# Optimization experiments

Hardware: AMD Instinct MI355X
Metric: run time of the kernel (lower is better)

## Reference

```python
import jax, jax.numpy as jnp
import numpy as np

B, N, D, H = 4, 1024, 1024, 16
Dh = D // H


def setup_inputs() -> dict:
    key = jax.random.key(0)
    ks = jax.random.split(key, 5)
    w = 0.02
    return {
        "x": jax.random.normal(ks[0], (B, N, D), dtype=jnp.float32),
        "Wq": jax.random.normal(ks[1], (D, D), dtype=jnp.float32) * w,
        "bq": jnp.zeros((D,), dtype=jnp.float32),
        "Wk": jax.random.normal(ks[2], (D, D), dtype=jnp.float32) * w,
        "bk": jnp.zeros((D,), dtype=jnp.float32),
        "Wv": jax.random.normal(ks[3], (D, D), dtype=jnp.float32) * w,
        "bv": jnp.zeros((D,), dtype=jnp.float32),
        "Wc": jax.random.normal(ks[4], (D, D), dtype=jnp.float32) * w,
        "bc": jnp.zeros((D,), dtype=jnp.float32),
    }


def reference(x, Wq, bq, Wk, bk, Wv, bv, Wc, bc):
    # q/k/v projections: nn.Linear computes x @ W.T + b
    q = jnp.einsum("bnd,ed->bne", x, Wq) + bq
    k = jnp.einsum("bnd,ed->bne", x, Wk) + bk
    v = jnp.einsum("bnd,ed->bne", x, Wv) + bv
    # split heads: [B,N,D] -> [B,H,N,Dh]
    qh = q.reshape(B, N, H, Dh).transpose(0, 2, 1, 3)
    kh = k.reshape(B, N, H, Dh).transpose(0, 2, 1, 3)
    vh = v.reshape(B, N, H, Dh).transpose(0, 2, 1, 3)
    # NOTE (faithful quirk): original uses scale = q.size(1) = seq_len N,
    # not head_dim, so scores are scaled by N**-0.5.
    scale = jnp.float32(N) ** -0.5
    scores = jnp.einsum("bhnd,bhmd->bhnm", qh, kh) * scale  # [B,H,N,N]
    attn = jax.nn.softmax(scores, axis=-1)
    # attn_dropout = 0.0 -> identity
    o = jnp.einsum("bhnm,bhmd->bhnd", attn, vh)  # [B,H,N,Dh]
    # NOTE (faithful quirk): original does v.resize(original_size) on the
    # contiguous [B,H,N,Dh] tensor, reinterpreting memory as [B,N,D]
    # WITHOUT permuting heads back. Replicate exactly:
    o = o.reshape(B, N, D)
    out = jnp.einsum("bnd,ed->bne", o, Wc) + bc
    return out
```

## Files before the change

### kernel.cpp

```cpp
#include <hip/hip_runtime.h>
#include <cstddef>
#include <cstdint>

#define B_  4
#define N_  1024
#define D_  1024
#define H_  16
#define DH  64
#define M_  4096

#define SC2 0.04508422f

typedef __attribute__((ext_vector_type(4)))  float   f32x4;
typedef __attribute__((ext_vector_type(16))) float   f32x16;
typedef __attribute__((ext_vector_type(8)))  __bf16  bf16x8;
typedef __attribute__((ext_vector_type(4)))  unsigned int u32x4;

#define MFMA(a, b, c)   __builtin_amdgcn_mfma_f32_16x16x32_bf16((a), (b), (c), 0, 0, 0)
#define MFMA32(a, b, c) __builtin_amdgcn_mfma_f32_32x32x16_bf16((a), (b), (c), 0, 0, 0)
#define GLDS(gp, lp) __builtin_amdgcn_global_load_lds( \
    (__attribute__((address_space(1))) void*)(gp),     \
    (__attribute__((address_space(3))) void*)(lp), 16, 0, 0)

static __device__ __forceinline__ unsigned cvtpk(float lo, float hi) {
    unsigned r;
    asm("v_cvt_pk_bf16_f32 %0, %1, %2" : "=v"(r) : "v"(lo), "v"(hi));
    return r;
}

__global__ __launch_bounds__(256) void convert_k(
    const float* __restrict__ x,  const float* __restrict__ Wq,
    const float* __restrict__ Wk, const float* __restrict__ Wv,
    const float* __restrict__ Wc,
    __bf16* __restrict__ xb, __bf16* __restrict__ wqkvb,
    __bf16* __restrict__ wcb)
{
    const unsigned u = blockIdx.x * 256u + threadIdx.x;
    const unsigned e = u * 8u;
    const float* src;
    __bf16* dst;
    if (e < 4194304u) { src = x + e; dst = xb + e; }
    else {
        const unsigned t2 = e - 4194304u;
        const unsigned wsel = t2 >> 20;
        const unsigned wo = t2 & 1048575u;
        src = (wsel == 0 ? Wq : wsel == 1 ? Wk : wsel == 2 ? Wv : Wc) + wo;
        dst = (wsel < 3 ? wqkvb + (size_t)wsel * 1048576u : wcb) + wo;
    }
    const float4 f0 = *(const float4*)(src);
    const float4 f1 = *(const float4*)(src + 4);
    bf16x8 r;
    r[0] = (__bf16)f0.x; r[1] = (__bf16)f0.y; r[2] = (__bf16)f0.z; r[3] = (__bf16)f0.w;
    r[4] = (__bf16)f1.x; r[5] = (__bf16)f1.y; r[6] = (__bf16)f1.z; r[7] = (__bf16)f1.w;
    *(bf16x8*)dst = r;
}

__global__ __launch_bounds__(512, 2) void gemm_qkv256(
    const __bf16* __restrict__ xb, const __bf16* __restrict__ Wb,
    const float* __restrict__ bq, const float* __restrict__ bk,
    const float* __restrict__ bv,
    __bf16* __restrict__ qk_out, __bf16* __restrict__ vT)
{
    __shared__ __bf16 ring[65536];

    const int tid  = threadIdx.x;
    const int w    = tid >> 6;
    const int lane = tid & 63;
    const int quad = lane >> 4;
    const int l15  = lane & 15;
    const int wr   = w >> 2;
    const int wc   = w & 3;

    const int bid = blockIdx.x;
    const bool VT = (bid >= 128);
    const int xcd = bid & 7;
    int m0, n0;
    const __bf16 *Ap, *Bp;
    if (!VT) {
        const int i  = bid >> 3;
        const int mt = (xcd >> 1) * 4 + (i >> 2);
        const int nt = (xcd & 1) * 4 + (i & 3);
        m0 = mt * 256; n0 = nt * 256;
        Ap = xb; Bp = Wb;
    } else {
        const int i  = (bid - 128) >> 3;
        m0 = (i & 3) * 256;
        n0 = (xcd * 2 + (i >> 2)) * 256;
        Ap = Wb + (size_t)2 * D_ * D_; Bp = xb;
    }

    const size_t sgl = (size_t)(w * 16 + l15) * D_ + quad * 8;
    const __bf16* Asrc = Ap + (size_t)m0 * D_ + sgl;
    const __bf16* Bsrc = Bp + (size_t)n0 * D_ + sgl;
    __bf16* const ringA = ring;
    __bf16* const ringB = ring + 32768;
    const int sdst = w * 1024;

#define STG_A(tt, h) do {                                               \
    const __bf16* s_ = Asrc + (size_t)(h) * 128 * D_ + (tt) * 64;       \
    __bf16* d_ = ringA + ((((tt) & 1) * 2 + (h)) * 8192) + sdst;        \
    GLDS(s_, d_); GLDS(s_ + 32, d_ + 512); } while (0)
#define STG_B(tt, h) do {                                               \
    const __bf16* s_ = Bsrc + (size_t)(h) * 128 * D_ + (tt) * 64;       \
    __bf16* d_ = ringB + ((((tt) & 1) * 2 + (h)) * 8192) + sdst;        \
    GLDS(s_, d_); GLDS(s_ + 32, d_ + 512); } while (0)

    f32x4 acc[8][4];
    #pragma unroll
    for (int i = 0; i < 8; ++i)
        #pragma unroll
        for (int j = 0; j < 4; ++j)
            acc[i][j] = (f32x4){0.f, 0.f, 0.f, 0.f};

    STG_B(0, 0); STG_B(0, 1);
    STG_A(0, 0); STG_A(0, 1);
    STG_B(1, 0); STG_B(1, 1);

    const int rdo = lane * 8;

#define READ_A(q)                                                       \
    afr[0][0] = *(const bf16x8*)(Asl + ((2*(q)  )*2 + 0)*512);          \
    afr[0][1] = *(const bf16x8*)(Asl + ((2*(q)  )*2 + 1)*512);          \
    afr[1][0] = *(const bf16x8*)(Asl + ((2*(q)+1)*2 + 0)*512);          \
    afr[1][1] = *(const bf16x8*)(Asl + ((2*(q)+1)*2 + 1)*512);

#define PHASE_MFMA(q)                                                   \
    __builtin_amdgcn_s_barrier();                                       \
    asm volatile("s_waitcnt lgkmcnt(0)" ::: "memory");                  \
    __builtin_amdgcn_s_setprio(1);                                      \
    _Pragma("unroll")                                                   \
    for (int i = 0; i < 2; ++i)                                         \
      _Pragma("unroll")                                                 \
      for (int nt = 0; nt < 4; ++nt) {                                  \
        acc[2*(q)+i][nt] = MFMA(afr[i][0], bfr[nt][0], acc[2*(q)+i][nt]); \
        acc[2*(q)+i][nt] = MFMA(afr[i][1], bfr[nt][1], acc[2*(q)+i][nt]); \
      }                                                                 \
    __builtin_amdgcn_s_setprio(0);

    for (int t = 0; t < 16; ++t) {
        if (t < 15) asm volatile("s_waitcnt vmcnt(4)" ::: "memory");
        else        asm volatile("s_waitcnt vmcnt(0)" ::: "memory");
        __builtin_amdgcn_s_barrier();

        const __bf16* Asl = ringA + ((t & 1) * 2 + wr) * 8192 + rdo;
        const __bf16* Bsl = ringB + ((t & 1) * 2 + (wc >> 1)) * 8192
                                  + (wc & 1) * 4096 + rdo;
        bf16x8 afr[2][2], bfr[4][2];

        if (t < 15) { STG_A(t + 1, 0); STG_A(t + 1, 1); }
        #pragma unroll
        for (int nt = 0; nt < 4; ++nt) {
            bfr[nt][0] = *(const bf16x8*)(Bsl + (nt * 2 + 0) * 512);
            bfr[nt][1] = *(const bf16x8*)(Bsl + (nt * 2 + 1) * 512);
        }
        READ_A(0)
        PHASE_MFMA(0)
        __builtin_amdgcn_s_barrier();

        if (t < 14) STG_B(t + 2, 0);
        READ_A(1)
        PHASE_MFMA(1)
        __builtin_amdgcn_s_barrier();

        if (t < 14) STG_B(t + 2, 1);
        READ_A(2)
        PHASE_MFMA(2)
        __builtin_amdgcn_s_barrier();

        READ_A(3)
        PHASE_MFMA(3)
    }
#undef STG_A
#undef STG_B
#undef READ_A
#undef PHASE_MFMA

    if (!VT) {
        const int zq = n0 >> 10;
        const float* bias = zq ? bk : bq;
        const float qs = zq ? 1.0f : SC2;
        const int nb = (n0 & 1023) + wc * 64;
        float bvv[4];
        #pragma unroll
        for (int nt = 0; nt < 4; ++nt) bvv[nt] = bias[nb + nt * 16 + l15];
        __bf16* C = qk_out + (size_t)zq * M_ * D_;
        #pragma unroll
        for (int mt = 0; mt < 8; ++mt) {
            #pragma unroll
            for (int r = 0; r < 4; ++r) {
                const int row = m0 + wr * 128 + mt * 16 + quad * 4 + r;
                #pragma unroll
                for (int nt = 0; nt < 4; ++nt) {
                    const int col = nb + nt * 16 + l15;
                    const size_t idx = (((size_t)(row >> 10) * H_ + (col >> 6)) * N_
                                        + (row & 1023)) * DH + (col & 63);
                    C[idx] = (__bf16)((acc[mt][nt][r] + bvv[nt]) * qs);
                }
            }
        }
    } else {
        #pragma unroll
        for (int mt = 0; mt < 8; ++mt) {
            #pragma unroll
            for (int r = 0; r < 4; ++r) {
                const int row = m0 + wr * 128 + mt * 16 + quad * 4 + r;
                const float brow = bv[row];
                #pragma unroll
                for (int nt = 0; nt < 4; ++nt) {
                    const int col = n0 + wc * 64 + nt * 16 + l15;
                    const size_t idx = (((size_t)(col >> 10) * H_ + (row >> 6)) * DH
                                        + (row & 63)) * N_ + (col & 1023);
                    vT[idx] = (__bf16)(acc[mt][nt][r] + brow);
                }
            }
        }
    }
}

__global__ __launch_bounds__(256, 6) void gemm_out(
    const __bf16* __restrict__ A0, const __bf16* __restrict__ Wb,
    const float* __restrict__ b0, float* __restrict__ Cb)
{
    __shared__ __bf16 As[2048];
    __shared__ __bf16 Bs[4096];

    const int tid  = threadIdx.x;
    const int w    = tid >> 6;
    const int lane = tid & 63;
    const int quad = lane >> 4;
    const int l15  = lane & 15;
    const int wr   = w >> 1, wc = w & 1;

    const int m0 = blockIdx.y * 64;
    const int n0 = blockIdx.x * 128;

    const int Tt = tid >> 6, ko = (tid >> 4) & 3, l = tid & 15;
    const size_t aoff  = (size_t)(m0 + Tt * 16 + l) * D_ + ko * 8;
    const size_t boff1 = (size_t)(n0 + Tt * 16 + l) * D_ + ko * 8;
    const size_t boff2 = boff1 + (size_t)64 * D_;
    __bf16* adst  = As + w * 512;
    __bf16* bdst1 = Bs + w * 512;
    __bf16* bdst2 = Bs + 2048 + w * 512;

    f32x4 acc[2][4];
    #pragma unroll
    for (int i = 0; i < 2; ++i)
        #pragma unroll
        for (int j = 0; j < 4; ++j)
            acc[i][j] = (f32x4){0.f, 0.f, 0.f, 0.f};

    for (int k0 = 0; k0 < D_; k0 += 32) {
        GLDS(A0 + aoff  + k0, adst);
        GLDS(Wb + boff1 + k0, bdst1);
        GLDS(Wb + boff2 + k0, bdst2);
        __syncthreads();

        bf16x8 af[2], bf[4];
        #pragma unroll
        for (int mt = 0; mt < 2; ++mt)
            af[mt] = *(const bf16x8*)(As + (((wr * 2 + mt) * 4 + quad) * 16 + l15) * 8);
        #pragma unroll
        for (int nt = 0; nt < 4; ++nt)
            bf[nt] = *(const bf16x8*)(Bs + (((wc * 4 + nt) * 4 + quad) * 16 + l15) * 8);
        #pragma unroll
        for (int mt = 0; mt < 2; ++mt)
            #pragma unroll
            for (int nt = 0; nt < 4; ++nt)
                acc[mt][nt] = MFMA(af[mt], bf[nt], acc[mt][nt]);
        __syncthreads();
    }

    float bvv[4];
    #pragma unroll
    for (int nt = 0; nt < 4; ++nt)
        bvv[nt] = b0[n0 + wc * 64 + nt * 16 + l15];
    #pragma unroll
    for (int mt = 0; mt < 2; ++mt) {
        #pragma unroll
        for (int r = 0; r < 4; ++r) {
            const int row = m0 + (wr * 2 + mt) * 16 + quad * 4 + r;
            #pragma unroll
            for (int nt = 0; nt < 4; ++nt) {
                const int col = n0 + wc * 64 + nt * 16 + l15;
                Cb[(size_t)row * D_ + col] = acc[mt][nt][r] + bvv[nt];
            }
        }
    }
}

__global__ __launch_bounds__(256, 2) void attn_mfma(
    const __bf16* __restrict__ qh, const __bf16* __restrict__ kh,
    const __bf16* __restrict__ vT, __bf16* __restrict__ ob)
{
    __shared__ __align__(16) __bf16 Ks[4096];
    __shared__ __align__(16) __bf16 Vs[4096];

    const int tid  = threadIdx.x;
    const int w    = tid >> 6;
    const int lane = tid & 63;
    const int la31 = lane & 31;
    const int hi   = lane >> 5;

    const int bh = blockIdx.x >> 3;
    const int qt = blockIdx.x & 7;
    const int b  = bh >> 4;
    const int h  = bh & 15;

    const size_t headQ = (size_t)(b * H_ + h) * N_;

    const int qrow = qt * 128 + w * 32 + la31;
    const __bf16* qp = qh + (headQ + qrow) * DH + hi * 8;
    const bf16x8 qf0 = *(const bf16x8*)(qp);
    const bf16x8 qf1 = *(const bf16x8*)(qp + 16);
    const bf16x8 qf2 = *(const bf16x8*)(qp + 32);
    const bf16x8 qf3 = *(const bf16x8*)(qp + 48);

    const __bf16* khead = kh + headQ * DH;
    const __bf16* vhead = vT + (size_t)(b * H_ + h) * DH * N_;

    const size_t koff0 = (size_t)la31 * DH + w * 16 + hi * 8;
    const size_t koff1 = koff0 + (size_t)32 * DH;
    const size_t voff0 = (size_t)((w & 1) * 32 + la31) * N_ + (w >> 1) * 16 + hi * 8;
    const size_t voff1 = voff0 + 32;
    __bf16* const kd0 = Ks + tid * 8;
    __bf16* const kd1 = Ks + tid * 8 + 2048;
    __bf16* const vd0 = Vs + tid * 8;
    __bf16* const vd1 = Vs + tid * 8 + 2048;

    f32x16 Ov0, Ov1;
    #pragma unroll
    for (int r = 0; r < 16; ++r) { Ov0[r] = 0.f; Ov1[r] = 0.f; }
    float psum = 0.f;

    bf16x8 kr0 = *(const bf16x8*)(khead + koff0);
    bf16x8 kr1 = *(const bf16x8*)(khead + koff1);
    bf16x8 vr0 = *(const bf16x8*)(vhead + voff0);
    bf16x8 vr1 = *(const bf16x8*)(vhead + voff1);

#define PACK(earr, base, dst) do {                                        \
    unsigned U_ = cvtpk(earr[(base) + 0], earr[(base) + 1]);              \
    unsigned W_ = cvtpk(earr[(base) + 2], earr[(base) + 3]);              \
    unsigned V_ = cvtpk(earr[(base) + 4], earr[(base) + 5]);              \
    unsigned Z_ = cvtpk(earr[(base) + 6], earr[(base) + 7]);              \
    asm volatile("v_permlane32_swap_b32 %0, %1" : "+v"(U_), "+v"(V_));    \
    asm volatile("v_permlane32_swap_b32 %0, %1" : "+v"(W_), "+v"(Z_));    \
    u32x4 pw_ = {U_, W_, V_, Z_};                                         \
    dst = __builtin_bit_cast(bf16x8, pw_);                                \
} while (0)

    for (int kt = 0; kt < 16; ++kt) {
        asm volatile("s_waitcnt lgkmcnt(0)" ::: "memory");
        __builtin_amdgcn_s_barrier();
        __builtin_amdgcn_sched_barrier(0);

        *(bf16x8*)kd0 = kr0;
        *(bf16x8*)kd1 = kr1;
        *(bf16x8*)vd0 = vr0;
        *(bf16x8*)vd1 = vr1;
        if (kt < 15) {
            const __bf16* kp = khead + (size_t)(kt + 1) * 64 * DH;
            const __bf16* vp = vhead + (size_t)(kt + 1) * 64;
            kr0 = *(const bf16x8*)(kp + koff0);
            kr1 = *(const bf16x8*)(kp + koff1);
            vr0 = *(const bf16x8*)(vp + voff0);
            vr1 = *(const bf16x8*)(vp + voff1);
        }
        asm volatile("s_waitcnt lgkmcnt(0)" ::: "memory");
        __builtin_amdgcn_s_barrier();
        __builtin_amdgcn_sched_barrier(0);

        f32x16 sa0, sa1;
        __builtin_amdgcn_s_setprio(1);
        {
            f32x16 z;
            #pragma unroll
            for (int r = 0; r < 16; ++r) z[r] = 0.f;
            bf16x8 kf;
            kf = *(const bf16x8*)(Ks + 0 * 512 + lane * 8); sa0 = MFMA32(kf, qf0, z);
            kf = *(const bf16x8*)(Ks + 1 * 512 + lane * 8); sa0 = MFMA32(kf, qf1, sa0);
            kf = *(const bf16x8*)(Ks + 2 * 512 + lane * 8); sa0 = MFMA32(kf, qf2, sa0);
            kf = *(const bf16x8*)(Ks + 3 * 512 + lane * 8); sa0 = MFMA32(kf, qf3, sa0);
            kf = *(const bf16x8*)(Ks + 4 * 512 + lane * 8); sa1 = MFMA32(kf, qf0, z);
            kf = *(const bf16x8*)(Ks + 5 * 512 + lane * 8); sa1 = MFMA32(kf, qf1, sa1);
            kf = *(const bf16x8*)(Ks + 6 * 512 + lane * 8); sa1 = MFMA32(kf, qf2, sa1);
            kf = *(const bf16x8*)(Ks + 7 * 512 + lane * 8); sa1 = MFMA32(kf, qf3, sa1);
        }
        __builtin_amdgcn_s_setprio(0);

        float e0[16], e1[16];
        #pragma unroll
        for (int r = 0; r < 16; ++r) { e0[r] = __builtin_exp2f(sa0[r]); psum += e0[r]; }
        #pragma unroll
        for (int r = 0; r < 16; ++r) { e1[r] = __builtin_exp2f(sa1[r]); psum += e1[r]; }

        bf16x8 pf0, pf1, pf2, pf3;
        PACK(e0, 0, pf0);
        PACK(e0, 8, pf1);
        PACK(e1, 0, pf2);
        PACK(e1, 8, pf3);

        __builtin_amdgcn_s_setprio(1);
        {
            bf16x8 vf;
            vf = *(const bf16x8*)(Vs + 0 * 512 + lane * 8); Ov0 = MFMA32(pf0, vf, Ov0);
            vf = *(const bf16x8*)(Vs + 2 * 512 + lane * 8); Ov0 = MFMA32(pf1, vf, Ov0);
            vf = *(const bf16x8*)(Vs + 4 * 512 + lane * 8); Ov0 = MFMA32(pf2, vf, Ov0);
            vf = *(const bf16x8*)(Vs + 6 * 512 + lane * 8); Ov0 = MFMA32(pf3, vf, Ov0);
            vf = *(const bf16x8*)(Vs + 1 * 512 + lane * 8); Ov1 = MFMA32(pf0, vf, Ov1);
            vf = *(const bf16x8*)(Vs + 3 * 512 + lane * 8); Ov1 = MFMA32(pf1, vf, Ov1);
            vf = *(const bf16x8*)(Vs + 5 * 512 + lane * 8); Ov1 = MFMA32(pf2, vf, Ov1);
            vf = *(const bf16x8*)(Vs + 7 * 512 + lane * 8); Ov1 = MFMA32(pf3, vf, Ov1);
        }
        __builtin_amdgcn_s_setprio(0);
    }
#undef PACK

    psum += __shfl_xor(psum, 32);
    const float inv = 1.0f / psum;

    __bf16* const obase = ob + (headQ + qt * 128 + w * 32) * DH;
    #pragma unroll
    for (int r = 0; r < 16; ++r) {
        const int q_r = (r & 3) + 8 * (r >> 2) + 4 * hi;
        const float ivr = __shfl(inv, q_r);
        __bf16* op = obase + (size_t)q_r * DH + la31;
        op[0]  = (__bf16)(Ov0[r] * ivr);
        op[32] = (__bf16)(Ov1[r] * ivr);
    }
}

extern "C" void kernel_launch(void* const* d_in, const int* in_sizes, int n_in,
                              void* d_out, int out_size, void* d_ws, size_t ws_size,
                              hipStream_t stream) {
    const float* x  = (const float*)d_in[0];
    const float* Wq = (const float*)d_in[1];
    const float* bq = (const float*)d_in[2];
    const float* Wk = (const float*)d_in[3];
    const float* bk = (const float*)d_in[4];
    const float* Wv = (const float*)d_in[5];
    const float* bv = (const float*)d_in[6];
    const float* Wc = (const float*)d_in[7];
    const float* bc = (const float*)d_in[8];
    float* out = (float*)d_out;

    char* base = (char*)d_ws;
    __bf16* xb    = (__bf16*)(base);
    __bf16* wqkvb = (__bf16*)(base + (size_t)8  * 1048576);
    __bf16* wcb   = (__bf16*)(base + (size_t)14 * 1048576);
    __bf16* qkvb  = (__bf16*)(base + (size_t)16 * 1048576);
    __bf16* vTb   = (__bf16*)(base + (size_t)40 * 1048576);
    __bf16* obf   = (__bf16*)(base);

    __bf16* qhb = qkvb;
    __bf16* khb = qkvb + (size_t)M_ * D_;

    convert_k<<<dim3(4096), dim3(256), 0, stream>>>(
        x, Wq, Wk, Wv, Wc, xb, wqkvb, wcb);

    gemm_qkv256<<<dim3(192), dim3(512), 0, stream>>>(
        xb, wqkvb, bq, bk, bv, qkvb, vTb);

    attn_mfma<<<dim3(512), dim3(256), 0, stream>>>(qhb, khb, vTb, obf);

    gemm_out<<<dim3(8, 64, 1), dim3(256), 0, stream>>>(obf, wcb, bc, out);
}
```

Measured before the change: 185.0 us.

## Split attention KV range across two wave groups per block and merge partials

The attention kernel now launches 512 threads per block. Two groups of four waves each process half of the 1024 keys (split-K), and each group has its own K/V shared-memory buffers. At the end, the second group writes its partial O and row sums to shared memory, and the first group adds them, normalizes and stores the output. This halves the serial loop length per wave and raises the number of resident waves to hide latency, at the cost of more shared memory, a reduction step and extra barriers.

```diff
diff --git a/kernel.cpp b/kernel.cpp
--- a/kernel.cpp
+++ b/kernel.cpp
@@ -288,15 +288,17 @@
     }
 }
 
-__global__ __launch_bounds__(256, 2) void attn_mfma(
+__global__ __launch_bounds__(512, 4) void attn_mfma(
     const __bf16* __restrict__ qh, const __bf16* __restrict__ kh,
     const __bf16* __restrict__ vT, __bf16* __restrict__ ob)
 {
-    __shared__ __align__(16) __bf16 Ks[4096];
-    __shared__ __align__(16) __bf16 Vs[4096];
+    __shared__ __align__(16) float smem_f[8448];
+    __bf16* const smem16 = (__bf16*)smem_f;
 
     const int tid  = threadIdx.x;
     const int w    = tid >> 6;
+    const int qw   = w >> 1;
+    const int ks   = w & 1;
     const int lane = tid & 63;
     const int la31 = lane & 31;
     const int hi   = lane >> 5;
@@ -308,24 +310,27 @@
 
     const size_t headQ = (size_t)(b * H_ + h) * N_;
 
-    const int qrow = qt * 128 + w * 32 + la31;
+    const int qrow = qt * 128 + qw * 32 + la31;
     const __bf16* qp = qh + (headQ + qrow) * DH + hi * 8;
     const bf16x8 qf0 = *(const bf16x8*)(qp);
     const bf16x8 qf1 = *(const bf16x8*)(qp + 16);
     const bf16x8 qf2 = *(const bf16x8*)(qp + 32);
     const bf16x8 qf3 = *(const bf16x8*)(qp + 48);
 
-    const __bf16* khead = kh + headQ * DH;
-    const __bf16* vhead = vT + (size_t)(b * H_ + h) * DH * N_;
-
-    const size_t koff0 = (size_t)la31 * DH + w * 16 + hi * 8;
+    const __bf16* khead = kh + headQ * DH + (size_t)(ks * 512) * DH;
+    const __bf16* vhead = vT + (size_t)(b * H_ + h) * DH * N_ + ks * 512;
+
+    const size_t koff0 = (size_t)la31 * DH + qw * 16 + hi * 8;
     const size_t koff1 = koff0 + (size_t)32 * DH;
-    const size_t voff0 = (size_t)((w & 1) * 32 + la31) * N_ + (w >> 1) * 16 + hi * 8;
+    const size_t voff0 = (size_t)((qw & 1) * 32 + la31) * N_ + (qw >> 1) * 16 + hi * 8;
     const size_t voff1 = voff0 + 32;
-    __bf16* const kd0 = Ks + tid * 8;
-    __bf16* const kd1 = Ks + tid * 8 + 2048;
-    __bf16* const vd0 = Vs + tid * 8;
-    __bf16* const vd1 = Vs + tid * 8 + 2048;
+    __bf16* const KsS = smem16 + ks * 4096;
+    __bf16* const VsS = smem16 + 8192 + ks * 4096;
+    const int ltid = qw * 64 + lane;
+    __bf16* const kd0 = KsS + ltid * 8;
+    __bf16* const kd1 = KsS + ltid * 8 + 2048;
+    __bf16* const vd0 = VsS + ltid * 8;
+    __bf16* const vd1 = VsS + ltid * 8 + 2048;
 
     f32x16 Ov0, Ov1;
     #pragma unroll
@@ -348,7 +353,7 @@
     dst = __builtin_bit_cast(bf16x8, pw_);                                \
 } while (0)
 
-    for (int kt = 0; kt < 16; ++kt) {
+    for (int kt = 0; kt < 8; ++kt) {
         asm volatile("s_waitcnt lgkmcnt(0)" ::: "memory");
         __builtin_amdgcn_s_barrier();
         __builtin_amdgcn_sched_barrier(0);
@@ -357,7 +362,7 @@
         *(bf16x8*)kd1 = kr1;
         *(bf16x8*)vd0 = vr0;
         *(bf16x8*)vd1 = vr1;
-        if (kt < 15) {
+        if (kt < 7) {
             const __bf16* kp = khead + (size_t)(kt + 1) * 64 * DH;
             const __bf16* vp = vhead + (size_t)(kt + 1) * 64;
             kr0 = *(const bf16x8*)(kp + koff0);
@@ -376,14 +381,14 @@
             #pragma unroll
             for (int r = 0; r < 16; ++r) z[r] = 0.f;
             bf16x8 kf;
-            kf = *(const bf16x8*)(Ks + 0 * 512 + lane * 8); sa0 = MFMA32(kf, qf0, z);
-            kf = *(const bf16x8*)(Ks + 1 * 512 + lane * 8); sa0 = MFMA32(kf, qf1, sa0);
-            kf = *(const bf16x8*)(Ks + 2 * 512 + lane * 8); sa0 = MFMA32(kf, qf2, sa0);
-            kf = *(const bf16x8*)(Ks + 3 * 512 + lane * 8); sa0 = MFMA32(kf, qf3, sa0);
-            kf = *(const bf16x8*)(Ks + 4 * 512 + lane * 8); sa1 = MFMA32(kf, qf0, z);
-            kf = *(const bf16x8*)(Ks + 5 * 512 + lane * 8); sa1 = MFMA32(kf, qf1, sa1);
-            kf = *(const bf16x8*)(Ks + 6 * 512 + lane * 8); sa1 = MFMA32(kf, qf2, sa1);
-            kf = *(const bf16x8*)(Ks + 7 * 512 + lane * 8); sa1 = MFMA32(kf, qf3, sa1);
+            kf = *(const bf16x8*)(KsS - ks * 4096 + ks * 4096 + 0 * 512 + lane * 8); sa0 = MFMA32(kf, qf0, z);
+            kf = *(const bf16x8*)(KsS + 1 * 512 + lane * 8); sa0 = MFMA32(kf, qf1, sa0);
+            kf = *(const bf16x8*)(KsS + 2 * 512 + lane * 8); sa0 = MFMA32(kf, qf2, sa0);
+            kf = *(const bf16x8*)(KsS + 3 * 512 + lane * 8); sa0 = MFMA32(kf, qf3, sa0);
+            kf = *(const bf16x8*)(KsS + 4 * 512 + lane * 8); sa1 = MFMA32(kf, qf0, z);
+            kf = *(const bf16x8*)(KsS + 5 * 512 + lane * 8); sa1 = MFMA32(kf, qf1, sa1);
+            kf = *(const bf16x8*)(KsS + 6 * 512 + lane * 8); sa1 = MFMA32(kf, qf2, sa1);
+            kf = *(const bf16x8*)(KsS + 7 * 512 + lane * 8); sa1 = MFMA32(kf, qf3, sa1);
         }
         __builtin_amdgcn_s_setprio(0);
 
@@ -402,30 +407,45 @@
         __builtin_amdgcn_s_setprio(1);
         {
             bf16x8 vf;
-            vf = *(const bf16x8*)(Vs + 0 * 512 + lane * 8); Ov0 = MFMA32(pf0, vf, Ov0);
-            vf = *(const bf16x8*)(Vs + 2 * 512 + lane * 8); Ov0 = MFMA32(pf1, vf, Ov0);
-            vf = *(const bf16x8*)(Vs + 4 * 512 + lane * 8); Ov0 = MFMA32(pf2, vf, Ov0);
-            vf = *(const bf16x8*)(Vs + 6 * 512 + lane * 8); Ov0 = MFMA32(pf3, vf, Ov0);
-            vf = *(const bf16x8*)(Vs + 1 * 512 + lane * 8); Ov1 = MFMA32(pf0, vf, Ov1);
-            vf = *(const bf16x8*)(Vs + 3 * 512 + lane * 8); Ov1 = MFMA32(pf1, vf, Ov1);
-            vf = *(const bf16x8*)(Vs + 5 * 512 + lane * 8); Ov1 = MFMA32(pf2, vf, Ov1);
-            vf = *(const bf16x8*)(Vs + 7 * 512 + lane * 8); Ov1 = MFMA32(pf3, vf, Ov1);
+            vf = *(const bf16x8*)(VsS + 0 * 512 + lane * 8); Ov0 = MFMA32(pf0, vf, Ov0);
+            vf = *(const bf16x8*)(VsS + 2 * 512 + lane * 8); Ov0 = MFMA32(pf1, vf, Ov0);
+            vf = *(const bf16x8*)(VsS + 4 * 512 + lane * 8); Ov0 = MFMA32(pf2, vf, Ov0);
+            vf = *(const bf16x8*)(VsS + 6 * 512 + lane * 8); Ov0 = MFMA32(pf3, vf, Ov0);
+            vf = *(const bf16x8*)(VsS + 1 * 512 + lane * 8); Ov1 = MFMA32(pf0, vf, Ov1);
+            vf = *(const bf16x8*)(VsS + 3 * 512 + lane * 8); Ov1 = MFMA32(pf1, vf, Ov1);
+            vf = *(const bf16x8*)(VsS + 5 * 512 + lane * 8); Ov1 = MFMA32(pf2, vf, Ov1);
+            vf = *(const bf16x8*)(VsS + 7 * 512 + lane * 8); Ov1 = MFMA32(pf3, vf, Ov1);
         }
         __builtin_amdgcn_s_setprio(0);
     }
 #undef PACK
 
     psum += __shfl_xor(psum, 32);
-    const float inv = 1.0f / psum;
-
-    __bf16* const obase = ob + (headQ + qt * 128 + w * 32) * DH;
-    #pragma unroll
-    for (int r = 0; r < 16; ++r) {
-        const int q_r = (r & 3) + 8 * (r >> 2) + 4 * hi;
-        const float ivr = __shfl(inv, q_r);
-        __bf16* op = obase + (size_t)q_r * DH + la31;
-        op[0]  = (__bf16)(Ov0[r] * ivr);
-        op[32] = (__bf16)(Ov1[r] * ivr);
+
+    __syncthreads();
+    float* const Cb = smem_f;
+    const int cidx = (qw * 64 + lane) * 33;
+    if (ks) {
+        #pragma unroll
+        for (int r = 0; r < 16; ++r) { Cb[cidx + r] = Ov0[r]; Cb[cidx + 16 + r] = Ov1[r]; }
+        Cb[cidx + 32] = psum;
+    }
+    __syncthreads();
+    if (ks == 0) {
+        #pragma unroll
+        for (int r = 0; r < 16; ++r) { Ov0[r] += Cb[cidx + r]; Ov1[r] += Cb[cidx + 16 + r]; }
+        psum += Cb[cidx + 32];
+
+        const float inv = 1.0f / psum;
+        __bf16* const obase = ob + (headQ + qt * 128 + qw * 32) * DH;
+        #pragma unroll
+        for (int r = 0; r < 16; ++r) {
+            const int q_r = (r & 3) + 8 * (r >> 2) + 4 * hi;
+            const float ivr = __shfl(inv, q_r);
+            __bf16* op = obase + (size_t)q_r * DH + la31;
+            op[0]  = (__bf16)(Ov0[r] * ivr);
+            op[32] = (__bf16)(Ov1[r] * ivr);
+        }
     }
 }
 
@@ -460,7 +480,7 @@
     gemm_qkv256<<<dim3(192), dim3(512), 0, stream>>>(
         xb, wqkvb, bq, bk, bv, qkvb, vTb);
 
-    attn_mfma<<<dim3(512), dim3(256), 0, stream>>>(qhb, khb, vTb, obf);
+    attn_mfma<<<dim3(512), dim3(512), 0, stream>>>(qhb, khb, vTb, obf);
 
     gemm_out<<<dim3(8, 64, 1), dim3(256), 0, stream>>>(obf, wcb, bc, out);
 }
```

Result: slower. 190.5 us (+3.0%).
